# Kernel tuning notes

Measured on AMD Instinct MI355X. Metric: run time of the kernel, lower is better.

Reference implementation:

```python
import jax, jax.numpy as jnp
import numpy as np

EMBED_DIM = 256
NUM_HEADS = 8
NUM_QUERIES = 448
TEMPERATURE = 10000.0
SCALE = 100.0
EPS = 1e-5
B, N = 1, 512
NUM_CLASSES = 91


def box_rel_encoding(src_boxes, tgt_boxes, eps=EPS):
    # boxes: [B, N, 4] as (cx, cy, w, h)
    xy1, wh1 = src_boxes[..., :2], src_boxes[..., 2:]
    xy2, wh2 = tgt_boxes[..., :2], tgt_boxes[..., 2:]
    delta_xy = jnp.abs(xy1[..., :, None, :] - xy2[..., None, :, :])          # [B,N,N,2]
    delta_xy = jnp.log(delta_xy / (wh1[..., :, None, :] + eps) + 1.0)
    delta_wh = jnp.log((wh1[..., :, None, :] + eps) / (wh2[..., None, :, :] + eps))
    return jnp.concatenate([delta_xy, delta_wh], axis=-1)                    # [B,N,N,4]


def get_sine_pos_embed(pos, num_pos_feats, temperature=TEMPERATURE, scale=SCALE):
    # pos: [..., C]; returns [..., C * num_pos_feats]; exchange_xy=False
    dim_t = jnp.arange(num_pos_feats, dtype=pos.dtype)
    dim_t = temperature ** (2.0 * jnp.floor(dim_t / 2.0) / num_pos_feats)
    x = pos[..., None] * scale / dim_t                                        # [...,C,F]
    emb = jnp.stack([jnp.sin(x[..., 0::2]), jnp.cos(x[..., 1::2])], axis=-1)  # [...,C,F/2,2]
    emb = emb.reshape(x.shape)                                                # [...,C,F]
    return emb.reshape(pos.shape[:-1] + (pos.shape[-1] * num_pos_feats,))


def setup_inputs() -> dict:
    key = jax.random.key(0)
    ks = jax.random.split(key, 9)
    s = 0.02
    return {
        "src_boxes": jax.random.uniform(ks[0], (B, N, 4), jnp.float32, 0.05, 0.95),
        "pred_logits": jax.random.normal(ks[1], (B, N, NUM_CLASSES), jnp.float32),
        "rank_emb": jax.random.normal(ks[2], (NUM_QUERIES, EMBED_DIM), jnp.float32) * s,
        "pre_W": jax.random.normal(ks[3], (EMBED_DIM, EMBED_DIM), jnp.float32) * s,
        "pre_b": jax.random.normal(ks[4], (EMBED_DIM,), jnp.float32) * s,
        "post_W": jax.random.normal(ks[5], (EMBED_DIM, 2 * EMBED_DIM), jnp.float32) * s,
        "post_b": jax.random.normal(ks[6], (EMBED_DIM,), jnp.float32) * s,
        "attn_W": jax.random.normal(ks[7], (NUM_HEADS, EMBED_DIM), jnp.float32) * s,
        "attn_b": jax.random.normal(ks[8], (NUM_HEADS,), jnp.float32) * s,
        "layer_idx": 2,
    }


def reference(src_boxes, pred_logits, rank_emb, pre_W, pre_b, post_W, post_b, attn_W, attn_b, layer_idx):
    num_denoising = N - NUM_QUERIES
    # --- no-grad block: pairwise box relation + rank-ordered gather reorder ---
    base = box_rel_encoding(src_boxes, src_boxes)                            # [B,N,N,4]
    scores = jnp.max(jax.nn.sigmoid(pred_logits[:, num_denoising:]), axis=-1)  # [B,Q]
    order = jnp.argsort(-scores, axis=1)                                      # descending  [B,Q]
    rank_indices = jnp.broadcast_to(jnp.arange(N, dtype=order.dtype), (B, N))
    rank_indices = rank_indices.at[:, num_denoising:].set(order + num_denoising)
    nr = base[:, num_denoising:, num_denoising:]                              # [B,Q,Q,4]
    nr = jnp.take_along_axis(nr, order[:, :, None, None], axis=1)
    nr = jnp.take_along_axis(nr, order[:, None, :, None], axis=2)
    base = base.at[:, num_denoising:, num_denoising:].set(nr)
    base = jax.lax.stop_gradient(base)
    # --- sine positional embedding of relation: [B,N,N,EMBED_DIM] ---
    pos = get_sine_pos_embed(base, EMBED_DIM // 4)
    # --- rank-aware relation: embedding -> pre linear -> pairwise sum ---
    normal_rank = rank_emb @ pre_W.T + pre_b                                  # [Q,E]
    rank_rel = jnp.zeros((B, N, EMBED_DIM), src_boxes.dtype)
    rank_rel = rank_rel.at[:, num_denoising:].set(normal_rank[None])
    rank_rel = rank_rel[:, :, None, :] + rank_rel[:, None, :, :]              # [B,N,N,E]
    relation = jnp.concatenate([pos, rank_rel], axis=-1)                      # [B,N,N,2E]
    relation = relation @ post_W.T + post_b                                   # [B,N,N,E]
    attn = jax.nn.relu(relation @ attn_W.T + attn_b)                          # [B,N,N,H]
    attn = jnp.transpose(attn, (0, 3, 1, 2))                                  # [B,H,N,N]
    return attn, rank_indices
```

## Files before the change

### kernel.cpp

```cpp
#include <hip/hip_runtime.h>
#include <hip/hip_bf16.h>
#include <math.h>

#define NN 512
#define NQ 448
#define ND 64
#define NC 91
#define ED 256
#define NH 8

typedef __attribute__((ext_vector_type(8))) short bf16x8;
typedef __attribute__((ext_vector_type(4))) float f32x4;

struct FreqArg { float fr[32]; };

__device__ int   g_perm[NN];
__device__ float g_c0[NH];
__device__ float g_w2a[NH * ED];
__device__ float g_nr[NQ * ED];
__device__ __align__(16) unsigned short g_WB[8 * 64 * 8];

__device__ inline unsigned short f2bfbits(float x) {
    __hip_bfloat16 h = __float2bfloat16(x);
    union { __hip_bfloat16 b; unsigned short u; } cv; cv.b = h; return cv.u;
}

__global__ __launch_bounds__(512) void k1(const float* __restrict__ logits,
                                          const float* __restrict__ attn_W,
                                          const float* __restrict__ attn_b,
                                          const float* __restrict__ post_W,
                                          const float* __restrict__ post_b,
                                          const float* __restrict__ pre_W,
                                          const float* __restrict__ pre_b,
                                          const float* __restrict__ rank_emb,
                                          float* __restrict__ out2) {
    __shared__ float smem[NQ * 33];
    int bid = blockIdx.x, t = threadIdx.x;
    if (bid == 0) {
        float* sbuf = smem;
        float mm = -INFINITY;
        for (int ck = 0; ck < 3; ++ck) {
            int cbase = ck * 32;
            __syncthreads();
            for (int idx = t; idx < NQ * 32; idx += 512) {
                int q = idx >> 5, cl = idx & 31, c = cbase + cl;
                sbuf[q * 33 + cl] = (c < NC) ? logits[(size_t)(ND + q) * NC + c] : -INFINITY;
            }
            __syncthreads();
            if (t < NQ) {
#pragma unroll 8
                for (int c = 0; c < 32; ++c) mm = fmaxf(mm, sbuf[t * 33 + c]);
            }
        }
        __syncthreads();
        if (t < NQ) sbuf[t] = mm;
        __syncthreads();
        if (t < NQ) {
            float s1 = sbuf[t];
            int r1 = 0;
            for (int jq = 0; jq < NQ; ++jq) {
                float sj = sbuf[jq];
                r1 += ((sj > s1) || (sj == s1 && jq < t)) ? 1 : 0;
            }
            g_perm[ND + r1] = ND + t;
            out2[ND + r1] = (float)(ND + t);
        }
        if (t < ND) {
            g_perm[t] = t;
            out2[t] = (float)t;
        }
    } else if (bid == 1) {
        int h = t >> 6, lane = t & 63;
        float v = 0.f;
#pragma unroll
        for (int k = 0; k < 4; ++k) {
            int c = lane + 64 * k;
            v = fmaf(attn_W[h * ED + c], post_b[c], v);
        }
        for (int off = 32; off > 0; off >>= 1) v += __shfl_down(v, off, 64);
        if (lane == 0) g_c0[h] = attn_b[h] + v;
    } else if (bid < 66) {
        int f = bid - 2;
        int h = f >> 3, seg = f & 7;
        float* sAW  = smem;
        float* sRed = smem + 256;
        if (t < ED) sAW[t] = attn_W[h * ED + t];
        __syncthreads();
        int dl = t & 63, cg = t >> 6;
        float m = 0.f;
        const float* pw = post_W + (size_t)(cg * 32) * 512 + seg * 64 + dl;
#pragma unroll
        for (int ci = 0; ci < 32; ++ci) m = fmaf(sAW[cg * 32 + ci], pw[(size_t)ci * 512], m);
        sRed[cg * 64 + dl] = m;
        __syncthreads();
        if (t < 64) {
            float v = 0.f;
#pragma unroll
            for (int cg2 = 0; cg2 < 8; ++cg2) v += sRed[cg2 * 64 + t];
            if (seg < 4) {
                int g = seg, k = t >> 1, r = t & 1;
                int s = k >> 2, ii = ((k & 3) << 1) | r;
                g_WB[s * 512 + (g * 16 + h) * 8 + ii] = f2bfbits(v);
            } else {
                g_w2a[h * ED + (seg - 4) * 64 + t] = v;
            }
        }
        if (h == 0 && seg < 4 && t < 512) {
            int s = t >> 6, hh = 8 + ((t >> 3) & 7), ii = t & 7;
            g_WB[s * 512 + (seg * 16 + hh) * 8 + ii] = 0;
        }
    } else {
        int nb = bid - 66;
        int q0 = (nb >> 3) * 16, d0 = (nb & 7) * 32;
        float* sP = smem;
        float* sR = smem + 32 * 257;
        for (int v = t; v < 32 * 256; v += 512)
            sP[(v >> 8) * 257 + (v & 255)] = pre_W[(size_t)(d0 + (v >> 8)) * ED + (v & 255)];
        for (int v = t; v < 16 * 256; v += 512)
            sR[(v >> 8) * 257 + (v & 255)] = rank_emb[(size_t)(q0 + (v >> 8)) * ED + (v & 255)];
        __syncthreads();
        int q = t >> 5, dl = t & 31;
        float acc = pre_b[d0 + dl];
#pragma unroll 8
        for (int e = 0; e < 256; ++e) acc = fmaf(sR[q * 257 + e], sP[dl * 257 + e], acc);
        g_nr[(size_t)(q0 + q) * ED + d0 + dl] = acc;
    }
}

__global__ __launch_bounds__(256) void k2(const float* __restrict__ boxes,
                                          FreqArg fa,
                                          float* __restrict__ out) {
    __shared__ bf16x8 sWB[8][64];
    __shared__ float sW[NH * 260];
    __shared__ float sN[32 * 260];
    __shared__ float sAf[32][9];
    __shared__ int   sPerm[32];
    __shared__ float sC0[NH];
    int t = threadIdx.x, bid = blockIdx.x;
    int i0 = (bid >> 5) * 16, j0 = (bid & 31) * 16;

    ((uint4*)sWB)[t]       = ((const uint4*)g_WB)[t];
    ((uint4*)sWB)[t + 256] = ((const uint4*)g_WB)[t + 256];
    for (int v = t; v < 512; v += 256) {
        float4 w = ((const float4*)g_w2a)[v];
        *(float4*)(sW + (v >> 6) * 260 + (v & 63) * 4) = w;
    }
    for (int v = t; v < 2048; v += 256) {
        int row = v >> 6, c4 = v & 63;
        int pos = (row < 16) ? (i0 + row) : (j0 + (row - 16));
        int qq = (pos >= ND) ? (pos - ND) : 0;
        float4 w = ((const float4*)(g_nr + (size_t)qq * ED))[c4];
        *(float4*)(sN + row * 260 + c4 * 4) = w;
    }
    if (t < NH) sC0[t] = g_c0[t];
    if (t >= 32 && t < 48) sPerm[t - 32] = g_perm[i0 + (t - 32)];
    else if (t >= 48 && t < 64) sPerm[t - 32] = g_perm[j0 + (t - 48)];
    __syncthreads();

    {
        int rr = t >> 3, h = t & 7;
        int pos = (rr < 16) ? (i0 + rr) : (j0 + (rr - 16));
        float a = 0.f;
        if (pos >= ND) {
            const float* nrow = sN + rr * 260;
            const float* wrow = sW + h * 260;
#pragma unroll 8
            for (int e = 0; e < ED; ++e) a = fmaf(nrow[e], wrow[e], a);
        }
        sAf[rr][h] = a;
    }
    __syncthreads();

    int wv = t >> 6, lane = t & 63;
    int g = lane >> 4, r = lane & 15;
    bool jdn = (j0 < ND);
    int j = j0 + r;
    float4 b2p = ((const float4*)boxes)[j];
    float4 b2s = jdn ? b2p : ((const float4*)boxes)[sPerm[16 + r]];
    float4 cb4 = *(const float4*)(sC0 + (g & 1) * 4);
    const float eps = 1e-5f;

#pragma unroll
    for (int gi = 0; gi < 4; ++gi) {
        int iloc = wv * 4 + gi;
        int i = i0 + iloc;
        bool prm = (i >= ND) && !jdn;
        float4 b1 = ((const float4*)boxes)[prm ? sPerm[iloc] : i];
        float4 b2 = prm ? b2s : b2p;

        float ft;
        if (g == 0)      ft = logf(fabsf(b1.x - b2.x) / (b1.z + eps) + 1.0f);
        else if (g == 1) ft = logf(fabsf(b1.y - b2.y) / (b1.w + eps) + 1.0f);
        else if (g == 2) ft = logf((b1.z + eps) / (b2.z + eps));
        else             ft = logf((b1.w + eps) / (b2.w + eps));

        f32x4 acc = {0.f, 0.f, 0.f, 0.f};
#pragma unroll
        for (int s = 0; s < 8; ++s) {
            bf16x8 bfrag;
#pragma unroll
            for (int a = 0; a < 4; ++a) {
                float rev = ft * fa.fr[s * 4 + a];
                rev -= floorf(rev);
                float sv = __builtin_amdgcn_sinf(rev);
                float cv = __builtin_amdgcn_cosf(rev);
                bfrag[2 * a]     = (short)f2bfbits(sv);
                bfrag[2 * a + 1] = (short)f2bfbits(cv);
            }
            acc = __builtin_amdgcn_mfma_f32_16x16x32_bf16(sWB[s][lane], bfrag, acc, 0, 0, 0);
        }

        if (g < 2) {
            const float* cbp = (const float*)&cb4;
#pragma unroll
            for (int qq = 0; qq < 4; ++qq) {
                int h = g * 4 + qq;
                float v = acc[qq] + cbp[qq] + sAf[iloc][h] + sAf[16 + r][h];
                v = v > 0.f ? v : 0.f;
                out[(size_t)h * (NN * NN) + (size_t)i * NN + j] = v;
            }
        }
    }
}

extern "C" void kernel_launch(void* const* d_in, const int* in_sizes, int n_in,
                              void* d_out, int out_size, void* d_ws, size_t ws_size,
                              hipStream_t stream) {
    const float* boxes    = (const float*)d_in[0];
    const float* logits   = (const float*)d_in[1];
    const float* rank_emb = (const float*)d_in[2];
    const float* pre_W    = (const float*)d_in[3];
    const float* pre_b    = (const float*)d_in[4];
    const float* post_W   = (const float*)d_in[5];
    const float* post_b   = (const float*)d_in[6];
    const float* attn_W   = (const float*)d_in[7];
    const float* attn_b   = (const float*)d_in[8];
    float* out = (float*)d_out;

    k1<<<290, 512, 0, stream>>>(logits, attn_W, attn_b, post_W, post_b,
                                pre_W, pre_b, rank_emb,
                                out + (size_t)NH * NN * NN);

    FreqArg fa;
    for (int k = 0; k < 32; ++k)
        fa.fr[k] = (float)(100.0 / (2.0 * M_PI) / pow(10000.0, (double)k / 32.0));

    k2<<<1024, 256, 0, stream>>>(boxes, fa, out);
}
```

Baseline: 53.64 us.

## Precompute per-row rank attention terms once and simplify main relation kernel

The per-row rank contribution (nr·w2a for each head) moves into a small separate kernel that writes a global table once. Before, every main-kernel block recomputed it for its 32 rows from a 32x256 shared-memory tile. The main kernel drops that staging and the extra barrier, and each block now covers a single row i across 64 columns over 4096 blocks, reading the precomputed terms from global. In exchange it adds a kernel launch and gives up the reuse of b1 and the setup cost that came from processing 4 rows per wave.

Measured after the change: 46.33 us. 1.16x faster.

```diff
diff --git a/kernel.cpp b/kernel.cpp
--- a/kernel.cpp
+++ b/kernel.cpp
@@ -18,6 +18,7 @@
 __device__ float g_c0[NH];
 __device__ float g_w2a[NH * ED];
 __device__ float g_nr[NQ * ED];
+__device__ float g_afull[NN * NH];
 __device__ __align__(16) unsigned short g_WB[8 * 64 * 8];
 
 __device__ inline unsigned short f2bfbits(float x) {
@@ -127,98 +128,98 @@
     }
 }
 
-__global__ __launch_bounds__(256) void k2(const float* __restrict__ boxes,
-                                          FreqArg fa,
-                                          float* __restrict__ out) {
+#define SRD 264
+__global__ __launch_bounds__(256) void k2afull() {
+    __shared__ float sW[NH * SRD];
+    __shared__ float sN[8 * SRD];
+    int bid = blockIdx.x, t = threadIdx.x;
+    if (bid < 56) {
+        int q0 = bid * 8;
+        for (int v = t; v < 512; v += 256) {
+            float4 w = ((const float4*)g_w2a)[v];
+            *(float4*)(sW + (v >> 6) * SRD + (v & 63) * 4) = w;
+        }
+        for (int v = t; v < 512; v += 256) {
+            int row = v >> 6, c4 = v & 63;
+            float4 w = ((const float4*)(g_nr + (size_t)(q0 + row) * ED))[c4];
+            *(float4*)(sN + row * SRD + c4 * 4) = w;
+        }
+        __syncthreads();
+        int o = t >> 2, sub = t & 3;
+        int q = o >> 3, h = o & 7;
+        const float* nrow = sN + q * SRD;
+        const float* wrow = sW + h * SRD;
+        float a = 0.f;
+#pragma unroll
+        for (int k4 = 0; k4 < 16; ++k4) {
+            int e4 = sub + 4 * k4;
+            float4 x = *(const float4*)(nrow + e4 * 4);
+            float4 y = *(const float4*)(wrow + e4 * 4);
+            a = fmaf(x.x, y.x, a); a = fmaf(x.y, y.y, a);
+            a = fmaf(x.z, y.z, a); a = fmaf(x.w, y.w, a);
+        }
+        a += __shfl_xor(a, 1, 64);
+        a += __shfl_xor(a, 2, 64);
+        if (sub == 0) g_afull[(size_t)(ND + q0 + q) * NH + h] = a;
+    } else {
+        for (int v = t; v < ND * NH; v += 256) g_afull[v] = 0.f;
+    }
+}
+
+__global__ __launch_bounds__(256) void relation_main(const float* __restrict__ boxes,
+                                                     FreqArg fa,
+                                                     float* __restrict__ out) {
     __shared__ bf16x8 sWB[8][64];
-    __shared__ float sW[NH * 260];
-    __shared__ float sN[32 * 260];
-    __shared__ float sAf[32][9];
-    __shared__ int   sPerm[32];
-    __shared__ float sC0[NH];
-    int t = threadIdx.x, bid = blockIdx.x;
-    int i0 = (bid >> 5) * 16, j0 = (bid & 31) * 16;
-
+    int t = threadIdx.x;
     ((uint4*)sWB)[t]       = ((const uint4*)g_WB)[t];
     ((uint4*)sWB)[t + 256] = ((const uint4*)g_WB)[t + 256];
-    for (int v = t; v < 512; v += 256) {
-        float4 w = ((const float4*)g_w2a)[v];
-        *(float4*)(sW + (v >> 6) * 260 + (v & 63) * 4) = w;
-    }
-    for (int v = t; v < 2048; v += 256) {
-        int row = v >> 6, c4 = v & 63;
-        int pos = (row < 16) ? (i0 + row) : (j0 + (row - 16));
-        int qq = (pos >= ND) ? (pos - ND) : 0;
-        float4 w = ((const float4*)(g_nr + (size_t)qq * ED))[c4];
-        *(float4*)(sN + row * 260 + c4 * 4) = w;
-    }
-    if (t < NH) sC0[t] = g_c0[t];
-    if (t >= 32 && t < 48) sPerm[t - 32] = g_perm[i0 + (t - 32)];
-    else if (t >= 48 && t < 64) sPerm[t - 32] = g_perm[j0 + (t - 48)];
     __syncthreads();
 
-    {
-        int rr = t >> 3, h = t & 7;
-        int pos = (rr < 16) ? (i0 + rr) : (j0 + (rr - 16));
-        float a = 0.f;
-        if (pos >= ND) {
-            const float* nrow = sN + rr * 260;
-            const float* wrow = sW + h * 260;
-#pragma unroll 8
-            for (int e = 0; e < ED; ++e) a = fmaf(nrow[e], wrow[e], a);
-        }
-        sAf[rr][h] = a;
-    }
-    __syncthreads();
-
-    int wv = t >> 6, lane = t & 63;
+    int wave = t >> 6, lane = t & 63;
     int g = lane >> 4, r = lane & 15;
-    bool jdn = (j0 < ND);
-    int j = j0 + r;
-    float4 b2p = ((const float4*)boxes)[j];
-    float4 b2s = jdn ? b2p : ((const float4*)boxes)[sPerm[16 + r]];
-    float4 cb4 = *(const float4*)(sC0 + (g & 1) * 4);
+    int i = blockIdx.x >> 3;
+    int j = ((blockIdx.x & 7) << 6) + (wave << 4) + r;
+
+    int pi = i, pj = j;
+    if (i >= ND && j >= ND) { pi = g_perm[i]; pj = g_perm[j]; }
+    float4 b1 = ((const float4*)boxes)[pi];
+    float4 b2 = ((const float4*)boxes)[pj];
     const float eps = 1e-5f;
-
-#pragma unroll
-    for (int gi = 0; gi < 4; ++gi) {
-        int iloc = wv * 4 + gi;
-        int i = i0 + iloc;
-        bool prm = (i >= ND) && !jdn;
-        float4 b1 = ((const float4*)boxes)[prm ? sPerm[iloc] : i];
-        float4 b2 = prm ? b2s : b2p;
-
-        float ft;
-        if (g == 0)      ft = logf(fabsf(b1.x - b2.x) / (b1.z + eps) + 1.0f);
-        else if (g == 1) ft = logf(fabsf(b1.y - b2.y) / (b1.w + eps) + 1.0f);
-        else if (g == 2) ft = logf((b1.z + eps) / (b2.z + eps));
-        else             ft = logf((b1.w + eps) / (b2.w + eps));
-
-        f32x4 acc = {0.f, 0.f, 0.f, 0.f};
-#pragma unroll
-        for (int s = 0; s < 8; ++s) {
-            bf16x8 bfrag;
-#pragma unroll
-            for (int a = 0; a < 4; ++a) {
-                float rev = ft * fa.fr[s * 4 + a];
-                rev -= floorf(rev);
-                float sv = __builtin_amdgcn_sinf(rev);
-                float cv = __builtin_amdgcn_cosf(rev);
-                bfrag[2 * a]     = (short)f2bfbits(sv);
-                bfrag[2 * a + 1] = (short)f2bfbits(cv);
-            }
-            acc = __builtin_amdgcn_mfma_f32_16x16x32_bf16(sWB[s][lane], bfrag, acc, 0, 0, 0);
-        }
-
-        if (g < 2) {
-            const float* cbp = (const float*)&cb4;
-#pragma unroll
-            for (int qq = 0; qq < 4; ++qq) {
-                int h = g * 4 + qq;
-                float v = acc[qq] + cbp[qq] + sAf[iloc][h] + sAf[16 + r][h];
-                v = v > 0.f ? v : 0.f;
-                out[(size_t)h * (NN * NN) + (size_t)i * NN + j] = v;
-            }
+    float ft;
+    if (g == 0)      ft = logf(fabsf(b1.x - b2.x) / (b1.z + eps) + 1.0f);
+    else if (g == 1) ft = logf(fabsf(b1.y - b2.y) / (b1.w + eps) + 1.0f);
+    else if (g == 2) ft = logf((b1.z + eps) / (b2.z + eps));
+    else             ft = logf((b1.w + eps) / (b2.w + eps));
+
+    f32x4 acc = {0.f, 0.f, 0.f, 0.f};
+#pragma unroll
+    for (int s = 0; s < 8; ++s) {
+        bf16x8 bfrag;
+#pragma unroll
+        for (int a = 0; a < 4; ++a) {
+            float rev = ft * fa.fr[s * 4 + a];
+            rev -= floorf(rev);
+            float sv = __builtin_amdgcn_sinf(rev);
+            float cv = __builtin_amdgcn_cosf(rev);
+            bfrag[2 * a]     = (short)f2bfbits(sv);
+            bfrag[2 * a + 1] = (short)f2bfbits(cv);
+        }
+        acc = __builtin_amdgcn_mfma_f32_16x16x32_bf16(sWB[s][lane], bfrag, acc, 0, 0, 0);
+    }
+
+    if (g < 2) {
+        float4 cb = *(const float4*)(g_c0 + g * 4);
+        float4 ai = *(const float4*)(g_afull + i * NH + g * 4);
+        float4 aj = *(const float4*)(g_afull + j * NH + g * 4);
+        const float* cbp = (const float*)&cb;
+        const float* aip = (const float*)&ai;
+        const float* ajp = (const float*)&aj;
+#pragma unroll
+        for (int q = 0; q < 4; ++q) {
+            int h = g * 4 + q;
+            float v = acc[q] + cbp[q] + aip[q] + ajp[q];
+            v = v > 0.f ? v : 0.f;
+            out[(size_t)h * (NN * NN) + i * NN + j] = v;
         }
     }
 }
@@ -240,10 +241,11 @@
     k1<<<290, 512, 0, stream>>>(logits, attn_W, attn_b, post_W, post_b,
                                 pre_W, pre_b, rank_emb,
                                 out + (size_t)NH * NN * NN);
+    k2afull<<<57, 256, 0, stream>>>();
 
     FreqArg fa;
     for (int k = 0; k < 32; ++k)
         fa.fr[k] = (float)(100.0 / (2.0 * M_PI) / pow(10000.0, (double)k / 32.0));
 
-    k2<<<1024, 256, 0, stream>>>(boxes, fa, out);
-}
+    relation_main<<<4096, 256, 0, stream>>>(boxes, fa, out);
+}
```
